# Kernel tuning notes

Measured on AMD Instinct MI355X. Metric: run time of the kernel, lower is better.

## Reference

```python
import jax, jax.numpy as jnp
import numpy as np

H = 64
EPS = 1e-8


def _quat_mul(q1, q2):
    w1, x1, y1, z1 = q1[..., 0], q1[..., 1], q1[..., 2], q1[..., 3]
    w2, x2, y2, z2 = q2[..., 0], q2[..., 1], q2[..., 2], q2[..., 3]
    return jnp.stack([
        w1 * w2 - x1 * x2 - y1 * y2 - z1 * z2,
        w1 * x2 + x1 * w2 + y1 * z2 - z1 * y2,
        w1 * y2 - x1 * z2 + y1 * w2 + z1 * x2,
        w1 * z2 + x1 * y2 - y1 * x2 + z1 * w2,
    ], axis=-1)


def _quat_conj(q):
    return q * jnp.array([1.0, -1.0, -1.0, -1.0], dtype=q.dtype)


def _oct_mul(o1, o2):
    # Cayley-Dickson: (a,b)(c,d) = (ac - conj(d) b, d a + b conj(c))
    a, b = o1[..., :4], o1[..., 4:]
    c, d = o2[..., :4], o2[..., 4:]
    re = _quat_mul(a, c) - _quat_mul(_quat_conj(d), b)
    im = _quat_mul(d, a) + _quat_mul(b, _quat_conj(c))
    return jnp.concatenate([re, im], axis=-1)


def setup_inputs() -> dict:
    key = jax.random.key(0)
    k0, k1, k2, k3, k4 = jax.random.split(key, 5)
    B, N, D = 16, 4096, H * 8
    o = jax.random.normal(k0, (B, N, D), dtype=jnp.float32)
    # scalar_mlp: Linear(2,32) -> GELU -> Linear(32,3), torch layout (out, in)
    W1 = jax.random.normal(k1, (32, 2), dtype=jnp.float32) * (1.0 / np.sqrt(2.0))
    b1 = jax.random.normal(k2, (32,), dtype=jnp.float32) * 0.01
    W2 = jax.random.normal(k3, (3, 32), dtype=jnp.float32) * (1.0 / np.sqrt(32.0))
    b2 = jax.random.normal(k4, (3,), dtype=jnp.float32) * 0.01
    alpha = jnp.asarray(0.25, dtype=jnp.float32)
    return {"o": o, "W1": W1, "b1": b1, "W2": W2, "b2": b2, "alpha": alpha}


def reference(o, W1, b1, W2, b2, alpha):
    B, N, D = o.shape
    oh = o.reshape(B, N, H, 8)                       # [B,N,H,8]
    r = oh[..., 0]                                   # real part [B,N,H]
    n = jnp.linalg.norm(oh[..., 1:], axis=-1)        # ||imag|| [B,N,H]
    inv = jnp.stack([r, n], axis=-1)                 # [B,N,H,2]
    h = jax.nn.gelu(inv @ W1.T + b1, approximate=False)
    scalars = h @ W2.T + b2                          # [B,N,H,3]
    a, b, c = scalars[..., 0], scalars[..., 1], scalars[..., 2]
    o2 = _oct_mul(oh, oh)
    o3 = _oct_mul(oh, o2)
    upd = a[..., None] * oh + b[..., None] * o2 + c[..., None] * o3
    upd = upd / jnp.maximum(jnp.linalg.norm(upd, axis=-1, keepdims=True), EPS)
    upd = upd.reshape(B, N, D)
    lam = jax.nn.sigmoid(alpha)
    return (1.0 - lam) * o + lam * upd
```

## Files before the change

kernel.cpp:

```cpp
#include <hip/hip_runtime.h>
#include <math.h>

#define OCT_EPS 1e-8f

__device__ __forceinline__ float fast_erf(float x) {
    float z = fabsf(x);
    float t = __builtin_amdgcn_rcpf(fmaf(0.3275911f, z, 1.0f));
    float p = fmaf(1.061405429f, t, -1.453152027f);
    p = fmaf(p, t, 1.421413741f);
    p = fmaf(p, t, -0.284496736f);
    p = fmaf(p, t, 0.254829592f);
    p = p * t;
    float e = __expf(-z * z);
    float r = fmaf(-p, e, 1.0f);
    return copysignf(r, x);
}

__device__ __forceinline__ float gelu_exact(float x) {
    return 0.5f * x * (1.0f + fast_erf(x * 0.70710678118654752f));
}

__global__ __launch_bounds__(256) void g2_ffn_kernel(
    const float* __restrict__ o,
    const float* __restrict__ W1,
    const float* __restrict__ b1,
    const float* __restrict__ W2,
    const float* __restrict__ b2,
    const float* __restrict__ alpha_p,
    float* __restrict__ out,
    int n_oct)
{
    int i = blockIdx.x * blockDim.x + threadIdx.x;
    if (i >= n_oct) return;

    const float4* ip = (const float4*)o;
    float4 lo = ip[2 * (size_t)i];
    float4 hi = ip[2 * (size_t)i + 1];

    float w = lo.x;
    float n2 = lo.y * lo.y;
    n2 = fmaf(lo.z, lo.z, n2);
    n2 = fmaf(lo.w, lo.w, n2);
    n2 = fmaf(hi.x, hi.x, n2);
    n2 = fmaf(hi.y, hi.y, n2);
    n2 = fmaf(hi.z, hi.z, n2);
    n2 = fmaf(hi.w, hi.w, n2);
    float n = __builtin_amdgcn_sqrtf(n2);
    float s = fmaf(w, w, n2);

    float a_acc = b2[0];
    float b_acc = b2[1];
    float c_acc = b2[2];
#pragma unroll
    for (int j = 0; j < 32; ++j) {
        float pre = fmaf(W1[2 * j], w, fmaf(W1[2 * j + 1], n, b1[j]));
        float h = gelu_exact(pre);
        a_acc = fmaf(W2[j], h, a_acc);
        b_acc = fmaf(W2[32 + j], h, b_acc);
        c_acc = fmaf(W2[64 + j], h, c_acc);
    }

    float alpha_c = fmaf(2.0f * b_acc, w, a_acc) + c_acc * fmaf(4.0f * w, w, -s);
    float beta_c  = -s * fmaf(2.0f * c_acc, w, b_acc);

    float t2 = fmaf(alpha_c * alpha_c, s,
               fmaf(2.0f * alpha_c * beta_c, w, beta_c * beta_c));
    float nrm = __builtin_amdgcn_sqrtf(t2);
    float inv = __builtin_amdgcn_rcpf(fmaxf(nrm, OCT_EPS));

    float alpha_in = alpha_p[0];
    float lam = 1.0f / (1.0f + __expf(-alpha_in));
    float oml = 1.0f - lam;

    float la = lam * alpha_c * inv;
    float lb = lam * beta_c * inv;

    float4 r0, r1;
    r0.x = fmaf(oml, lo.x, fmaf(la, lo.x, lb));
    r0.y = fmaf(oml, lo.y, la * lo.y);
    r0.z = fmaf(oml, lo.z, la * lo.z);
    r0.w = fmaf(oml, lo.w, la * lo.w);
    r1.x = fmaf(oml, hi.x, la * hi.x);
    r1.y = fmaf(oml, hi.y, la * hi.y);
    r1.z = fmaf(oml, hi.z, la * hi.z);
    r1.w = fmaf(oml, hi.w, la * hi.w);

    float4* op = (float4*)out;
    op[2 * (size_t)i]     = r0;
    op[2 * (size_t)i + 1] = r1;
}

extern "C" void kernel_launch(void* const* d_in, const int* in_sizes, int n_in,
                              void* d_out, int out_size, void* d_ws, size_t ws_size,
                              hipStream_t stream) {
    const float* o     = (const float*)d_in[0];
    const float* W1    = (const float*)d_in[1];
    const float* b1    = (const float*)d_in[2];
    const float* W2    = (const float*)d_in[3];
    const float* b2    = (const float*)d_in[4];
    const float* alpha = (const float*)d_in[5];
    float* out = (float*)d_out;

    int n_oct = in_sizes[0] / 8;
    int block = 256;
    int grid = (n_oct + block - 1) / block;
    g2_ffn_kernel<<<grid, block, 0, stream>>>(o, W1, b1, W2, b2, alpha, out, n_oct);
}
```

Baseline: 246.9 us.

## Process two octonions per thread with packed float2 math and folded GELU constants

Each thread now handles two octonions, one from each half of the array, and runs the scalar MLP with 2-wide vector types so the compiler can emit packed FMA instructions. The GELU is rewritten around exp2 with the erf scaling, the 0.5 factor and log2(e) folded into constants, and the final scale is applied once to the accumulators. This is meant to cut VALU instruction count in a kernel that is bound by transcendental math. In exchange the thread count halves and register pressure rises, and an odd octonion count would leave the last element unprocessed.

```diff
diff --git a/kernel.cpp b/kernel.cpp
--- a/kernel.cpp
+++ b/kernel.cpp
@@ -3,22 +3,13 @@
 
 #define OCT_EPS 1e-8f
 
-__device__ __forceinline__ float fast_erf(float x) {
-    float z = fabsf(x);
-    float t = __builtin_amdgcn_rcpf(fmaf(0.3275911f, z, 1.0f));
-    float p = fmaf(1.061405429f, t, -1.453152027f);
-    p = fmaf(p, t, 1.421413741f);
-    p = fmaf(p, t, -0.284496736f);
-    p = fmaf(p, t, 0.254829592f);
-    p = p * t;
-    float e = __expf(-z * z);
-    float r = fmaf(-p, e, 1.0f);
-    return copysignf(r, x);
+typedef float v2f __attribute__((ext_vector_type(2)));
+
+static __device__ __forceinline__ v2f splat(float x) { v2f r; r.x = x; r.y = x; return r; }
+static __device__ __forceinline__ v2f fma2(v2f a, v2f b, v2f c) {
+    return __builtin_elementwise_fma(a, b, c);
 }
 
-__device__ __forceinline__ float gelu_exact(float x) {
-    return 0.5f * x * (1.0f + fast_erf(x * 0.70710678118654752f));
-}
 
 __global__ __launch_bounds__(256) void g2_ffn_kernel(
     const float* __restrict__ o,
@@ -28,66 +19,95 @@
     const float* __restrict__ b2,
     const float* __restrict__ alpha_p,
     float* __restrict__ out,
-    int n_oct)
+    int half)
 {
     int i = blockIdx.x * blockDim.x + threadIdx.x;
-    if (i >= n_oct) return;
+    if (i >= half) return;
+    size_t i0 = (size_t)i;
+    size_t i1 = i0 + (size_t)half;
 
     const float4* ip = (const float4*)o;
-    float4 lo = ip[2 * (size_t)i];
-    float4 hi = ip[2 * (size_t)i + 1];
+    float4 lo0 = ip[2 * i0];
+    float4 hi0 = ip[2 * i0 + 1];
+    float4 lo1 = ip[2 * i1];
+    float4 hi1 = ip[2 * i1 + 1];
 
-    float w = lo.x;
-    float n2 = lo.y * lo.y;
-    n2 = fmaf(lo.z, lo.z, n2);
-    n2 = fmaf(lo.w, lo.w, n2);
-    n2 = fmaf(hi.x, hi.x, n2);
-    n2 = fmaf(hi.y, hi.y, n2);
-    n2 = fmaf(hi.z, hi.z, n2);
-    n2 = fmaf(hi.w, hi.w, n2);
-    float n = __builtin_amdgcn_sqrtf(n2);
-    float s = fmaf(w, w, n2);
+    v2f wv = { lo0.x, lo1.x };
+    v2f c1 = { lo0.y, lo1.y }, c2 = { lo0.z, lo1.z }, c3 = { lo0.w, lo1.w };
+    v2f c4 = { hi0.x, hi1.x }, c5 = { hi0.y, hi1.y }, c6 = { hi0.z, hi1.z }, c7 = { hi0.w, hi1.w };
 
-    float a_acc = b2[0];
-    float b_acc = b2[1];
-    float c_acc = b2[2];
+    v2f n2 = c1 * c1;
+    n2 = fma2(c2, c2, n2);
+    n2 = fma2(c3, c3, n2);
+    n2 = fma2(c4, c4, n2);
+    n2 = fma2(c5, c5, n2);
+    n2 = fma2(c6, c6, n2);
+    n2 = fma2(c7, c7, n2);
+    v2f nv = { __builtin_amdgcn_sqrtf(n2.x), __builtin_amdgcn_sqrtf(n2.y) };
+    v2f sv = fma2(wv, wv, n2);
+
+    const float C_  = 0.84932185f;
+    const float K1_ = 0.2727374f;
+    const float KF_ = 0.5887050f;
+
+    v2f accA = splat(0.0f), accB = splat(0.0f), accC = splat(0.0f);
 #pragma unroll
     for (int j = 0; j < 32; ++j) {
-        float pre = fmaf(W1[2 * j], w, fmaf(W1[2 * j + 1], n, b1[j]));
-        float h = gelu_exact(pre);
-        a_acc = fmaf(W2[j], h, a_acc);
-        b_acc = fmaf(W2[32 + j], h, b_acc);
-        c_acc = fmaf(W2[64 + j], h, c_acc);
+        v2f pre = fma2(splat(W1[2 * j]), wv,
+                  fma2(splat(W1[2 * j + 1]), nv, splat(b1[j])));
+        v2f x2 = pre * splat(C_);
+        v2f z2 = x2 * x2;
+        v2f e  = { exp2f(-z2.x), exp2f(-z2.y) };
+        v2f ax = { __builtin_fabsf(x2.x), __builtin_fabsf(x2.y) };
+        v2f den = fma2(splat(K1_), ax, splat(1.0f));
+        v2f t  = { __builtin_amdgcn_rcpf(den.x), __builtin_amdgcn_rcpf(den.y) };
+        v2f p  = fma2(splat(1.061405429f), t, splat(-1.453152027f));
+        p = fma2(p, t, splat(1.421413741f));
+        p = fma2(p, t, splat(-0.284496736f));
+        p = fma2(p, t, splat(0.254829592f));
+        v2f pt = p * t;
+        v2f m  = fma2(-pt, e, splat(1.0f));
+        v2f g  = fma2(ax, m, x2);
+        accA = fma2(splat(W2[j]),      g, accA);
+        accB = fma2(splat(W2[32 + j]), g, accB);
+        accC = fma2(splat(W2[64 + j]), g, accC);
     }
 
-    float alpha_c = fmaf(2.0f * b_acc, w, a_acc) + c_acc * fmaf(4.0f * w, w, -s);
-    float beta_c  = -s * fmaf(2.0f * c_acc, w, b_acc);
+    v2f av = fma2(splat(KF_), accA, splat(b2[0]));
+    v2f bv = fma2(splat(KF_), accB, splat(b2[1]));
+    v2f cv = fma2(splat(KF_), accC, splat(b2[2]));
 
-    float t2 = fmaf(alpha_c * alpha_c, s,
-               fmaf(2.0f * alpha_c * beta_c, w, beta_c * beta_c));
-    float nrm = __builtin_amdgcn_sqrtf(t2);
-    float inv = __builtin_amdgcn_rcpf(fmaxf(nrm, OCT_EPS));
+    v2f q       = fma2(splat(4.0f) * wv, wv, -sv);
+    v2f alpha_c = fma2(cv, q, fma2(bv + bv, wv, av));
+    v2f beta_c  = -(sv * fma2(cv + cv, wv, bv));
+
+    v2f ab = alpha_c * beta_c;
+    v2f t2 = fma2(alpha_c * alpha_c, sv, fma2(ab + ab, wv, beta_c * beta_c));
+    v2f nrm = { __builtin_amdgcn_sqrtf(t2.x), __builtin_amdgcn_sqrtf(t2.y) };
+    v2f inv = { __builtin_amdgcn_rcpf(fmaxf(nrm.x, OCT_EPS)),
+                __builtin_amdgcn_rcpf(fmaxf(nrm.y, OCT_EPS)) };
 
     float alpha_in = alpha_p[0];
     float lam = 1.0f / (1.0f + __expf(-alpha_in));
     float oml = 1.0f - lam;
 
-    float la = lam * alpha_c * inv;
-    float lb = lam * beta_c * inv;
+    v2f la = splat(lam) * (alpha_c * inv);
+    v2f lb = splat(lam) * (beta_c * inv);
+    v2f sc = splat(oml) + la;
 
-    float4 r0, r1;
-    r0.x = fmaf(oml, lo.x, fmaf(la, lo.x, lb));
-    r0.y = fmaf(oml, lo.y, la * lo.y);
-    r0.z = fmaf(oml, lo.z, la * lo.z);
-    r0.w = fmaf(oml, lo.w, la * lo.w);
-    r1.x = fmaf(oml, hi.x, la * hi.x);
-    r1.y = fmaf(oml, hi.y, la * hi.y);
-    r1.z = fmaf(oml, hi.z, la * hi.z);
-    r1.w = fmaf(oml, hi.w, la * hi.w);
+    v2f rw = fma2(sc, wv, lb);
+    v2f r1 = sc * c1, r2 = sc * c2, r3 = sc * c3;
+    v2f r4 = sc * c4, r5 = sc * c5, r6 = sc * c6, r7 = sc * c7;
 
     float4* op = (float4*)out;
-    op[2 * (size_t)i]     = r0;
-    op[2 * (size_t)i + 1] = r1;
+    float4 a0 = { rw.x, r1.x, r2.x, r3.x };
+    float4 a1 = { r4.x, r5.x, r6.x, r7.x };
+    float4 b0 = { rw.y, r1.y, r2.y, r3.y };
+    float4 b1o = { r4.y, r5.y, r6.y, r7.y };
+    op[2 * i0]     = a0;
+    op[2 * i0 + 1] = a1;
+    op[2 * i1]     = b0;
+    op[2 * i1 + 1] = b1o;
 }
 
 extern "C" void kernel_launch(void* const* d_in, const int* in_sizes, int n_in,
@@ -102,7 +122,8 @@
     float* out = (float*)d_out;
 
     int n_oct = in_sizes[0] / 8;
+    int half = n_oct >> 1;
     int block = 256;
-    int grid = (n_oct + block - 1) / block;
-    g2_ffn_kernel<<<grid, block, 0, stream>>>(o, W1, b1, W2, b2, alpha, out, n_oct);
+    int grid = (half + block - 1) / block;
+    g2_ffn_kernel<<<grid, block, 0, stream>>>(o, W1, b1, W2, b2, alpha, out, half);
 }
```

Result: no change. 248.3 us (+0.6%).

## Process two octonions per thread and fold GELU constants into pre-scaled erf

Applied to the files above, without the earlier changes.

Each thread now handles two octonions, one from each half of the array, so the per-j weight loads are shared and two independent dependency chains interleave for more ILP. The GELU/erf is refactored algebraically: the pre-activation is scaled once so exp2 can be used directly, the 0.5*x*(1+erf) is folded into |x|*(...)+x with the constant factor applied once after the accumulation. The final normalization uses rsq instead of sqrt+rcp, and the sigmoid uses exp2/rcp. This lowers ALU work per element but halves the thread count and assumes an even octonion count.

```diff
diff --git a/kernel.cpp b/kernel.cpp
--- a/kernel.cpp
+++ b/kernel.cpp
@@ -1,24 +1,6 @@
 #include <hip/hip_runtime.h>
 #include <math.h>
 
-#define OCT_EPS 1e-8f
-
-__device__ __forceinline__ float fast_erf(float x) {
-    float z = fabsf(x);
-    float t = __builtin_amdgcn_rcpf(fmaf(0.3275911f, z, 1.0f));
-    float p = fmaf(1.061405429f, t, -1.453152027f);
-    p = fmaf(p, t, 1.421413741f);
-    p = fmaf(p, t, -0.284496736f);
-    p = fmaf(p, t, 0.254829592f);
-    p = p * t;
-    float e = __expf(-z * z);
-    float r = fmaf(-p, e, 1.0f);
-    return copysignf(r, x);
-}
-
-__device__ __forceinline__ float gelu_exact(float x) {
-    return 0.5f * x * (1.0f + fast_erf(x * 0.70710678118654752f));
-}
 
 __global__ __launch_bounds__(256) void g2_ffn_kernel(
     const float* __restrict__ o,
@@ -28,66 +10,117 @@
     const float* __restrict__ b2,
     const float* __restrict__ alpha_p,
     float* __restrict__ out,
-    int n_oct)
+    int half)
 {
     int i = blockIdx.x * blockDim.x + threadIdx.x;
-    if (i >= n_oct) return;
+    if (i >= half) return;
+    size_t i0 = (size_t)i;
+    size_t i1 = i0 + (size_t)half;
 
     const float4* ip = (const float4*)o;
-    float4 lo = ip[2 * (size_t)i];
-    float4 hi = ip[2 * (size_t)i + 1];
+    float4 A0 = ip[2 * i0], A1 = ip[2 * i0 + 1];
+    float4 B0 = ip[2 * i1], B1 = ip[2 * i1 + 1];
 
-    float w = lo.x;
-    float n2 = lo.y * lo.y;
-    n2 = fmaf(lo.z, lo.z, n2);
-    n2 = fmaf(lo.w, lo.w, n2);
-    n2 = fmaf(hi.x, hi.x, n2);
-    n2 = fmaf(hi.y, hi.y, n2);
-    n2 = fmaf(hi.z, hi.z, n2);
-    n2 = fmaf(hi.w, hi.w, n2);
-    float n = __builtin_amdgcn_sqrtf(n2);
-    float s = fmaf(w, w, n2);
+    float wa = A0.x;
+    float na2 = A0.y * A0.y;
+    na2 = fmaf(A0.z, A0.z, na2);  na2 = fmaf(A0.w, A0.w, na2);
+    na2 = fmaf(A1.x, A1.x, na2);  na2 = fmaf(A1.y, A1.y, na2);
+    na2 = fmaf(A1.z, A1.z, na2);  na2 = fmaf(A1.w, A1.w, na2);
+    float nna = __builtin_amdgcn_sqrtf(na2);
+    float sa  = fmaf(wa, wa, na2);
 
-    float a_acc = b2[0];
-    float b_acc = b2[1];
-    float c_acc = b2[2];
+    float wb = B0.x;
+    float nb2 = B0.y * B0.y;
+    nb2 = fmaf(B0.z, B0.z, nb2);  nb2 = fmaf(B0.w, B0.w, nb2);
+    nb2 = fmaf(B1.x, B1.x, nb2);  nb2 = fmaf(B1.y, B1.y, nb2);
+    nb2 = fmaf(B1.z, B1.z, nb2);  nb2 = fmaf(B1.w, B1.w, nb2);
+    float nnb = __builtin_amdgcn_sqrtf(nb2);
+    float sb  = fmaf(wb, wb, nb2);
+
+    const float C_  = 0.84932180f;
+    const float K1_ = 0.2727375f;
+    const float KF_ = 0.5887050f;
+
+    float aA = 0.0f, aB = 0.0f, aC = 0.0f;
+    float bA = 0.0f, bB = 0.0f, bC = 0.0f;
+
 #pragma unroll
     for (int j = 0; j < 32; ++j) {
-        float pre = fmaf(W1[2 * j], w, fmaf(W1[2 * j + 1], n, b1[j]));
-        float h = gelu_exact(pre);
-        a_acc = fmaf(W2[j], h, a_acc);
-        b_acc = fmaf(W2[32 + j], h, b_acc);
-        c_acc = fmaf(W2[64 + j], h, c_acc);
+        float wr  = W1[2 * j];
+        float wn  = W1[2 * j + 1];
+        float bj  = b1[j];
+        float w2a = W2[j];
+        float w2b = W2[32 + j];
+        float w2c = W2[64 + j];
+
+        float xa = C_ * fmaf(wr, wa, fmaf(wn, nna, bj));
+        float xb = C_ * fmaf(wr, wb, fmaf(wn, nnb, bj));
+
+        float ea = __builtin_amdgcn_exp2f(-(xa * xa));
+        float eb = __builtin_amdgcn_exp2f(-(xb * xb));
+
+        float ta = __builtin_amdgcn_rcpf(fmaf(K1_, fabsf(xa), 1.0f));
+        float tb = __builtin_amdgcn_rcpf(fmaf(K1_, fabsf(xb), 1.0f));
+
+        float pa = fmaf(1.061405429f, ta, -1.453152027f);
+        float pb = fmaf(1.061405429f, tb, -1.453152027f);
+        pa = fmaf(pa, ta, 1.421413741f);   pb = fmaf(pb, tb, 1.421413741f);
+        pa = fmaf(pa, ta, -0.284496736f);  pb = fmaf(pb, tb, -0.284496736f);
+        pa = fmaf(pa, ta, 0.254829592f);   pb = fmaf(pb, tb, 0.254829592f);
+
+        float ga = fmaf(fabsf(xa), fmaf(-(pa * ta), ea, 1.0f), xa);
+        float gb = fmaf(fabsf(xb), fmaf(-(pb * tb), eb, 1.0f), xb);
+
+        aA = fmaf(w2a, ga, aA);   bA = fmaf(w2a, gb, bA);
+        aB = fmaf(w2b, ga, aB);   bB = fmaf(w2b, gb, bB);
+        aC = fmaf(w2c, ga, aC);   bC = fmaf(w2c, gb, bC);
     }
 
-    float alpha_c = fmaf(2.0f * b_acc, w, a_acc) + c_acc * fmaf(4.0f * w, w, -s);
-    float beta_c  = -s * fmaf(2.0f * c_acc, w, b_acc);
-
-    float t2 = fmaf(alpha_c * alpha_c, s,
-               fmaf(2.0f * alpha_c * beta_c, w, beta_c * beta_c));
-    float nrm = __builtin_amdgcn_sqrtf(t2);
-    float inv = __builtin_amdgcn_rcpf(fmaxf(nrm, OCT_EPS));
+    float avA = fmaf(KF_, aA, b2[0]);
+    float bvA = fmaf(KF_, aB, b2[1]);
+    float cvA = fmaf(KF_, aC, b2[2]);
+    float avB = fmaf(KF_, bA, b2[0]);
+    float bvB = fmaf(KF_, bB, b2[1]);
+    float cvB = fmaf(KF_, bC, b2[2]);
 
     float alpha_in = alpha_p[0];
-    float lam = 1.0f / (1.0f + __expf(-alpha_in));
+    float lam = __builtin_amdgcn_rcpf(
+        1.0f + __builtin_amdgcn_exp2f(-alpha_in * 1.44269504f));
     float oml = 1.0f - lam;
 
-    float la = lam * alpha_c * inv;
-    float lb = lam * beta_c * inv;
+    float qa  = fmaf(4.0f * wa, wa, -sa);
+    float ala = fmaf(cvA, qa, fmaf(bvA + bvA, wa, avA));
+    float bea = -(sa * fmaf(cvA + cvA, wa, bvA));
+    float t2a = fmaf(ala * bea, wa + wa, fmaf(ala * ala, sa, bea * bea));
+    float inva = __builtin_amdgcn_rsqf(fmaxf(t2a, 1e-16f));
+    float laa = lam * ala * inva;
+    float lba = lam * bea * inva;
+    float sca = oml + laa;
 
-    float4 r0, r1;
-    r0.x = fmaf(oml, lo.x, fmaf(la, lo.x, lb));
-    r0.y = fmaf(oml, lo.y, la * lo.y);
-    r0.z = fmaf(oml, lo.z, la * lo.z);
-    r0.w = fmaf(oml, lo.w, la * lo.w);
-    r1.x = fmaf(oml, hi.x, la * hi.x);
-    r1.y = fmaf(oml, hi.y, la * hi.y);
-    r1.z = fmaf(oml, hi.z, la * hi.z);
-    r1.w = fmaf(oml, hi.w, la * hi.w);
+    float4 ra0, ra1;
+    ra0.x = fmaf(sca, A0.x, lba);
+    ra0.y = sca * A0.y;  ra0.z = sca * A0.z;  ra0.w = sca * A0.w;
+    ra1.x = sca * A1.x;  ra1.y = sca * A1.y;  ra1.z = sca * A1.z;  ra1.w = sca * A1.w;
+
+    float qb  = fmaf(4.0f * wb, wb, -sb);
+    float alb = fmaf(cvB, qb, fmaf(bvB + bvB, wb, avB));
+    float beb = -(sb * fmaf(cvB + cvB, wb, bvB));
+    float t2b = fmaf(alb * beb, wb + wb, fmaf(alb * alb, sb, beb * beb));
+    float invb = __builtin_amdgcn_rsqf(fmaxf(t2b, 1e-16f));
+    float lab = lam * alb * invb;
+    float lbb = lam * beb * invb;
+    float scb = oml + lab;
+
+    float4 rb0, rb1;
+    rb0.x = fmaf(scb, B0.x, lbb);
+    rb0.y = scb * B0.y;  rb0.z = scb * B0.z;  rb0.w = scb * B0.w;
+    rb1.x = scb * B1.x;  rb1.y = scb * B1.y;  rb1.z = scb * B1.z;  rb1.w = scb * B1.w;
 
     float4* op = (float4*)out;
-    op[2 * (size_t)i]     = r0;
-    op[2 * (size_t)i + 1] = r1;
+    op[2 * i0]     = ra0;
+    op[2 * i0 + 1] = ra1;
+    op[2 * i1]     = rb0;
+    op[2 * i1 + 1] = rb1;
 }
 
 extern "C" void kernel_launch(void* const* d_in, const int* in_sizes, int n_in,
@@ -102,7 +135,8 @@
     float* out = (float*)d_out;
 
     int n_oct = in_sizes[0] / 8;
+    int half = n_oct >> 1;
     int block = 256;
-    int grid = (n_oct + block - 1) / block;
-    g2_ffn_kernel<<<grid, block, 0, stream>>>(o, W1, b1, W2, b2, alpha, out, n_oct);
+    int grid = (half + block - 1) / block;
+    g2_ffn_kernel<<<grid, block, 0, stream>>>(o, W1, b1, W2, b2, alpha, out, half);
 }
```

Result: no change. 247.8 us (+0.4%).
